# Performance work log

Hardware: AMD Instinct MI355X
Metric: run time of the kernel (lower is better)

Reference implementation:

```python
import jax, jax.numpy as jnp
import numpy as np

NUM_CLASSES = 91
BBOX_XFORM_CLIP = float(np.log(1000.0 / 16.0))
WX, WY, WW, WH = 10.0, 10.0, 5.0, 5.0  # torchvision BoxCoder weights
DETECTIONS_PER_IMG = 100


def _decode_boxes(reg, props):
    # reg: [P, 4*C], props: [P, 4] -> [P, C, 4]  (torchvision BoxCoder.decode)
    widths = props[:, 2] - props[:, 0]
    heights = props[:, 3] - props[:, 1]
    ctr_x = props[:, 0] + 0.5 * widths
    ctr_y = props[:, 1] + 0.5 * heights
    r = reg.reshape(reg.shape[0], -1, 4)
    dx = r[..., 0] / WX
    dy = r[..., 1] / WY
    dw = jnp.minimum(r[..., 2] / WW, BBOX_XFORM_CLIP)
    dh = jnp.minimum(r[..., 3] / WH, BBOX_XFORM_CLIP)
    pcx = dx * widths[:, None] + ctr_x[:, None]
    pcy = dy * heights[:, None] + ctr_y[:, None]
    pw = jnp.exp(dw) * widths[:, None]
    ph = jnp.exp(dh) * heights[:, None]
    return jnp.stack([pcx - 0.5 * pw, pcy - 0.5 * ph, pcx + 0.5 * pw, pcy + 0.5 * ph], axis=-1)


def _clip_boxes(boxes, h, w):
    x = jnp.clip(boxes[..., 0::2], 0.0, float(w))
    y = jnp.clip(boxes[..., 1::2], 0.0, float(h))
    return jnp.stack([x[..., 0], y[..., 0], x[..., 1], y[..., 1]], axis=-1)


def setup_inputs() -> dict:
    key = jax.random.key(0)
    k1, k2, k3, k4, k5 = jax.random.split(key, 5)
    B, P, C, FD = 8, 4096, NUM_CLASSES, 1024
    N = B * P
    class_logits = jax.random.normal(k1, (N, C), dtype=jnp.float32)
    box_regression = 0.5 * jax.random.normal(k2, (N, 4 * C), dtype=jnp.float32)
    # valid proposal boxes inside an 800x800 image: x1<x2, y1<y2
    xy = jax.random.uniform(k3, (N, 2), dtype=jnp.float32) * 700.0
    wh = jax.random.uniform(k4, (N, 2), dtype=jnp.float32) * 96.0 + 4.0
    proposals = jnp.concatenate([xy, xy + wh], axis=-1)
    box_features = jax.random.normal(k5, (N, FD), dtype=jnp.float32)
    return {"class_logits": class_logits, "box_regression": box_regression,
            "proposals": proposals, "box_features": box_features,
            "batch_size": B, "image_h": 800, "image_w": 800}


def reference(class_logits, box_regression, proposals, box_features, batch_size, image_h, image_w):
    B = int(batch_size)
    N = class_logits.shape[0]
    P = N // B
    lg = class_logits.reshape(B, P, NUM_CLASSES)
    rg = box_regression.reshape(B, P, 4 * NUM_CLASSES)
    pr = proposals.reshape(B, P, 4)
    ft = box_features.reshape(B, P, -1)

    def per_image(lg_i, rg_i, pr_i, ft_i):
        boxes = _decode_boxes(rg_i, pr_i)            # [P, C, 4]
        scores = jax.nn.softmax(lg_i, axis=-1)       # [P, C]
        boxes = _clip_boxes(boxes, image_h, image_w)
        boxes = boxes[:, 1:].reshape(-1, 4)          # drop background class -> [P*(C-1), 4]
        scores = scores[:, 1:].reshape(-1)
        # batched_nms with iou_threshold=1.0 never suppresses anything (IoU<=1 always),
        # so keep == indices sorted by score descending, truncated to detections_per_img.
        keep = jnp.argsort(-scores)[:DETECTIONS_PER_IMG]
        boxes = boxes / float(image_h)               # source divides by image_shape[0] only
        kept_boxes = boxes[keep]                     # [D, 4]
        feat_idx = keep // (NUM_CLASSES - 1)         # source: keep / (num_classes-1) int div
        kept_feats = ft_i[feat_idx]                  # [D, FD]
        return kept_boxes, kept_feats

    all_boxes, all_features = jax.vmap(per_image)(lg, rg, pr, ft)
    return all_boxes, all_features
```

## Files before the change

kernel.cpp:

```cpp
#include <hip/hip_runtime.h>
#include <hip/hip_bf16.h>

#define NCLS 91
#define NFG 90
#define NDET 100
#define FDIM 1024
#define CAP 4096
#define NBUK 4096
#define BBOX_CLIP 4.135166556742356f
#define K1_TPB 256
#define RPB 32
#define K2_TPB 1024

__global__ __launch_bounds__(K1_TPB) void k1_soft(
        const float* __restrict__ logits, float* __restrict__ rowoff,
        unsigned* __restrict__ maxk, int N) {
    int wave = threadIdx.x >> 6, lane = threadIdx.x & 63;
    int rowbase = blockIdx.x * RPB + wave * (RPB / 4);
    for (int it = 0; it < RPB / 4; it++) {
        long long row = rowbase + it;
        if (row >= N) return;
        const float* r = logits + row * NCLS;
        float l1 = r[lane];
        float l2 = (lane < NCLS - 64) ? r[64 + lane] : -INFINITY;
        float mf = fmaxf((lane == 0) ? -INFINITY : l1, l2);
        #pragma unroll
        for (int o = 32; o; o >>= 1) mf = fmaxf(mf, __shfl_xor(mf, o));
        float m = fmaxf(mf, __shfl(l1, 0));
        float e = expf(l1 - m) + ((lane < NCLS - 64) ? expf(l2 - m) : 0.0f);
        #pragma unroll
        for (int o = 32; o; o >>= 1) e += __shfl_xor(e, o);
        float off = m + logf(e);
        unsigned km = __float_as_uint(expf(mf - off));
        if (lane == 0) { rowoff[row] = off; maxk[row] = km; }
    }
}

__device__ __forceinline__ void find_threshold(const unsigned* hist,
                                               unsigned* wsum, unsigned* sh_lb,
                                               int tid, unsigned target) {
    unsigned local[16]; unsigned s = 0, run = 0;
    if (tid < 256) {
        #pragma unroll
        for (int i = 0; i < 16; i++) { local[i] = hist[tid * 16 + i]; s += local[i]; }
        run = s;
        #pragma unroll
        for (int off = 1; off < 64; off <<= 1) {
            unsigned v = __shfl_down(run, off);
            if ((tid & 63) + off < 64) run += v;
        }
        if ((tid & 63) == 0) wsum[tid >> 6] = run;
    }
    __syncthreads();
    if (tid < 256) {
        int w = tid >> 6;
        #pragma unroll
        for (int ww = 0; ww < 4; ww++) if (ww > w) run += wsum[ww];
        unsigned above = run - s;
        #pragma unroll
        for (int i = 15; i >= 0; i--) {
            unsigned prev = above; above += local[i];
            if (above >= target && prev < target)
                *sh_lb = ((unsigned)(tid * 16 + i)) << 20;
        }
    }
    __syncthreads();
}

__global__ __launch_bounds__(K2_TPB) void k2_select(
        const float* __restrict__ logits, const float* __restrict__ reg,
        const float* __restrict__ props,
        const int* __restrict__ pH, const int* __restrict__ pW,
        const float* __restrict__ rowoff, const unsigned* __restrict__ maxk,
        float* __restrict__ outBoxes, unsigned* __restrict__ keepRow, int P) {
    __shared__ unsigned long long cand[CAP];
    __shared__ unsigned long long cbuf[2048];
    __shared__ unsigned hist[NBUK];
    __shared__ unsigned wsum[4];
    __shared__ unsigned sh_lb, sh_lb2, sh_nhot, sh_ncand, sh_n2;

    const int img = blockIdx.x;
    const int tid = threadIdx.x;
    const unsigned* mk = maxk + (size_t)img * P;
    unsigned* hot = (unsigned*)cbuf;

    if (tid == 0) { sh_nhot = 0; sh_ncand = 0; sh_n2 = 0; sh_lb = 0; sh_lb2 = 0; }
    for (int b = tid; b < NBUK; b += K2_TPB) hist[b] = 0u;
    __syncthreads();

    for (int r = tid; r < P; r += K2_TPB) atomicAdd(&hist[mk[r] >> 20], 1u);
    __syncthreads();
    find_threshold(hist, wsum, &sh_lb, tid, NDET);
    const unsigned lb = sh_lb;
    const unsigned lbh = lb ? lb - 1 : 0;

    for (int r = tid; r < P; r += K2_TPB)
        if (mk[r] >= lbh) hot[atomicAdd(&sh_nhot, 1u)] = (unsigned)r;
    __syncthreads();
    const int nhot = (int)sh_nhot;

    const int wave = tid >> 6, lane = tid & 63;
    for (int i = wave; i < nhot; i += K2_TPB / 64) {
        int rl = (int)hot[i];
        long long row = (long long)img * P + rl;
        float off = rowoff[row];
        const float* r = logits + row * NCLS;
        float l1 = r[lane];
        float l2 = (lane < NCLS - 64) ? r[64 + lane] : -INFINITY;
        if (lane >= 1) {
            unsigned k = __float_as_uint(expf(l1 - off));
            if (k >= lb) {
                unsigned pos = atomicAdd(&sh_ncand, 1u);
                if (pos < CAP)
                    cand[pos] = ((unsigned long long)k << 32) |
                                (unsigned)(0xFFFFFFFFu - (unsigned)(rl * NFG + lane - 1));
            }
        }
        if (lane < NCLS - 64) {
            unsigned k = __float_as_uint(expf(l2 - off));
            if (k >= lb) {
                unsigned pos = atomicAdd(&sh_ncand, 1u);
                if (pos < CAP)
                    cand[pos] = ((unsigned long long)k << 32) |
                                (unsigned)(0xFFFFFFFFu - (unsigned)(rl * NFG + 63 + lane));
            }
        }
    }
    __syncthreads();
    unsigned cnt = sh_ncand; if (cnt > CAP) cnt = CAP;
    int n;

    if (cnt > 128) {
        for (int b = tid; b < NBUK; b += K2_TPB) hist[b] = 0u;
        __syncthreads();
        for (int i = tid; i < (int)cnt; i += K2_TPB)
            atomicAdd(&hist[(unsigned)(cand[i] >> 52)], 1u);
        __syncthreads();
        find_threshold(hist, wsum, &sh_lb2, tid, NDET);
        unsigned lb2 = sh_lb2;
        for (int i = tid; i < (int)cnt; i += K2_TPB) {
            unsigned long long k64 = cand[i];
            if ((unsigned)(k64 >> 32) >= lb2) {
                unsigned pos = atomicAdd(&sh_n2, 1u);
                if (pos < 2048) cbuf[pos] = k64;
            }
        }
        __syncthreads();
        unsigned cnt2 = sh_n2;
        if (cnt2 <= 2048) {
            cnt = cnt2;
            n = 128; while (n < (int)cnt) n <<= 1;
            for (int i = tid; i < n; i += K2_TPB)
                cand[i] = (i < (int)cnt) ? cbuf[i] : 0ULL;
            __syncthreads();
        } else {
            n = 128; while (n < (int)cnt) n <<= 1;
            for (int i = tid; i < n; i += K2_TPB) if (i >= (int)cnt) cand[i] = 0ULL;
            __syncthreads();
        }
    } else {
        n = 128;
        for (int i = tid; i < n; i += K2_TPB) if (i >= (int)cnt) cand[i] = 0ULL;
        __syncthreads();
    }

    for (int k = 2; k <= n; k <<= 1) {
        for (int j = k >> 1; j > 0; j >>= 1) {
            for (int i = tid; i < n; i += K2_TPB) {
                int ixj = i ^ j;
                if (ixj > i) {
                    bool up = ((i & k) == 0);
                    unsigned long long a = cand[i], b = cand[ixj];
                    if ((a > b) == up) { cand[i] = b; cand[ixj] = a; }
                }
            }
            __syncthreads();
        }
    }

    if (tid < NDET) {
        unsigned long long key = cand[n - 1 - tid];
        unsigned e = 0xFFFFFFFFu - (unsigned)(key & 0xFFFFFFFFull);
        int pr = e / NFG, cm = e - pr * NFG, c = cm + 1;
        long long rw = (long long)img * P + pr;
        float x1 = props[rw * 4 + 0], y1 = props[rw * 4 + 1];
        float x2 = props[rw * 4 + 2], y2 = props[rw * 4 + 3];
        float w = x2 - x1, hgt = y2 - y1;
        float cx = x1 + 0.5f * w, cy = y1 + 0.5f * hgt;
        const float* rr = reg + rw * (4 * NCLS) + 4 * c;
        float dx = rr[0] / 10.0f, dy = rr[1] / 10.0f;
        float dw = fminf(rr[2] / 5.0f, BBOX_CLIP);
        float dh = fminf(rr[3] / 5.0f, BBOX_CLIP);
        float pcx = dx * w + cx, pcy = dy * hgt + cy;
        float pw_ = expf(dw) * w, ph_ = expf(dh) * hgt;
        float bx1 = pcx - 0.5f * pw_, by1 = pcy - 0.5f * ph_;
        float bx2 = pcx + 0.5f * pw_, by2 = pcy + 0.5f * ph_;
        float W = (float)(*pW), H = (float)(*pH);
        bx1 = fminf(fmaxf(bx1, 0.0f), W);
        bx2 = fminf(fmaxf(bx2, 0.0f), W);
        by1 = fminf(fmaxf(by1, 0.0f), H);
        by2 = fminf(fmaxf(by2, 0.0f), H);
        int o = (img * NDET + tid) * 4;
        outBoxes[o + 0] = bx1 / H;
        outBoxes[o + 1] = by1 / H;
        outBoxes[o + 2] = bx2 / H;
        outBoxes[o + 3] = by2 / H;
        keepRow[img * NDET + tid] = (unsigned)rw;
    }
}

__global__ __launch_bounds__(256) void k3_feats(
        const float* __restrict__ feats, const unsigned* __restrict__ keepRow,
        float* __restrict__ outF) {
    int det = blockIdx.x;
    long long r = keepRow[det];
    const float4* src = (const float4*)(feats + r * FDIM);
    float4* dst = (float4*)(outF + (long long)det * FDIM);
    dst[threadIdx.x] = src[threadIdx.x];
}

extern "C" void kernel_launch(void* const* d_in, const int* in_sizes, int n_in,
                              void* d_out, int out_size, void* d_ws, size_t ws_size,
                              hipStream_t stream) {
    const float* logits = (const float*)d_in[0];
    const float* reg    = (const float*)d_in[1];
    const float* props  = (const float*)d_in[2];
    const float* feats  = (const float*)d_in[3];
    const int*   pH     = (const int*)d_in[5];
    const int*   pW     = (const int*)d_in[6];

    int N = in_sizes[0] / NCLS;
    int B = out_size / (NDET * (4 + FDIM));
    int P = N / B;

    char* ws = (char*)d_ws;
    float*    rowoff  = (float*)ws;
    unsigned* maxk    = (unsigned*)(rowoff + N);
    unsigned* keepRow = (unsigned*)(maxk + N);

    float* outBoxes = (float*)d_out;
    float* outFeats = outBoxes + (size_t)B * NDET * 4;

    k1_soft<<<(N + RPB - 1) / RPB, K1_TPB, 0, stream>>>(logits, rowoff, maxk, N);
    k2_select<<<B, K2_TPB, 0, stream>>>(logits, reg, props, pH, pW,
                                        rowoff, maxk, outBoxes, keepRow, P);
    k3_feats<<<B * NDET, 256, 0, stream>>>(feats, keepRow, outFeats);
}
```

Baseline: 224.2 us.

## Split per-image selection into multi-block collect and sort kernels with global histogram

The row-max histogram moves into the softmax kernel through global atomics, so the selection kernel no longer rebuilds it. Candidate collection is spread over 8 blocks per image that write into a global candidate buffer with global atomic counters. A separate per-image kernel then refines the threshold and sorts. This is meant to remove the serial per-image work done by only 8 blocks, at the cost of two extra launches (zeroing and the split), global atomics, and a candidate cap that can overflow.

```diff
diff --git a/kernel.cpp b/kernel.cpp
--- a/kernel.cpp
+++ b/kernel.cpp
@@ -1,20 +1,28 @@
 #include <hip/hip_runtime.h>
-#include <hip/hip_bf16.h>
 
 #define NCLS 91
 #define NFG 90
 #define NDET 100
 #define FDIM 1024
-#define CAP 4096
 #define NBUK 4096
+#define CAP_G 8192
+#define CAP_L 4096
+#define HOT_CAP 2048
 #define BBOX_CLIP 4.135166556742356f
 #define K1_TPB 256
 #define RPB 32
 #define K2_TPB 1024
+#define GPB 8
+
+__global__ __launch_bounds__(256) void k0_zero(unsigned* __restrict__ p, int n) {
+    int i = blockIdx.x * 256 + threadIdx.x;
+    if (i < n) p[i] = 0u;
+}
 
 __global__ __launch_bounds__(K1_TPB) void k1_soft(
         const float* __restrict__ logits, float* __restrict__ rowoff,
-        unsigned* __restrict__ maxk, int N) {
+        unsigned* __restrict__ maxk, unsigned* __restrict__ ghist,
+        int N, int P) {
     int wave = threadIdx.x >> 6, lane = threadIdx.x & 63;
     int rowbase = blockIdx.x * RPB + wave * (RPB / 4);
     for (int it = 0; it < RPB / 4; it++) {
@@ -32,7 +40,11 @@
         for (int o = 32; o; o >>= 1) e += __shfl_xor(e, o);
         float off = m + logf(e);
         unsigned km = __float_as_uint(expf(mf - off));
-        if (lane == 0) { rowoff[row] = off; maxk[row] = km; }
+        if (lane == 0) {
+            rowoff[row] = off; maxk[row] = km;
+            int img = (int)(row / P);
+            atomicAdd(&ghist[img * NBUK + (km >> 20)], 1u);
+        }
     }
 }
 
@@ -67,39 +79,36 @@
     __syncthreads();
 }
 
-__global__ __launch_bounds__(K2_TPB) void k2_select(
-        const float* __restrict__ logits, const float* __restrict__ reg,
-        const float* __restrict__ props,
-        const int* __restrict__ pH, const int* __restrict__ pW,
-        const float* __restrict__ rowoff, const unsigned* __restrict__ maxk,
-        float* __restrict__ outBoxes, unsigned* __restrict__ keepRow, int P) {
-    __shared__ unsigned long long cand[CAP];
-    __shared__ unsigned long long cbuf[2048];
-    __shared__ unsigned hist[NBUK];
+__global__ __launch_bounds__(K2_TPB) void k2a_collect(
+        const float* __restrict__ logits, const float* __restrict__ rowoff,
+        const unsigned* __restrict__ maxk, const unsigned* __restrict__ ghist,
+        unsigned long long* __restrict__ gcand, unsigned* __restrict__ gcnt,
+        int P) {
+    __shared__ unsigned hot[HOT_CAP];
     __shared__ unsigned wsum[4];
-    __shared__ unsigned sh_lb, sh_lb2, sh_nhot, sh_ncand, sh_n2;
-
-    const int img = blockIdx.x;
+    __shared__ unsigned sh_lb, sh_nhot;
+
+    const int img = blockIdx.x / GPB, sub = blockIdx.x % GPB;
     const int tid = threadIdx.x;
-    const unsigned* mk = maxk + (size_t)img * P;
-    unsigned* hot = (unsigned*)cbuf;
-
-    if (tid == 0) { sh_nhot = 0; sh_ncand = 0; sh_n2 = 0; sh_lb = 0; sh_lb2 = 0; }
-    for (int b = tid; b < NBUK; b += K2_TPB) hist[b] = 0u;
-    __syncthreads();
-
-    for (int r = tid; r < P; r += K2_TPB) atomicAdd(&hist[mk[r] >> 20], 1u);
-    __syncthreads();
-    find_threshold(hist, wsum, &sh_lb, tid, NDET);
+    if (tid == 0) { sh_lb = 0; sh_nhot = 0; }
+    find_threshold(ghist + (size_t)img * NBUK, wsum, &sh_lb, tid, NDET);
     const unsigned lb = sh_lb;
     const unsigned lbh = lb ? lb - 1 : 0;
 
-    for (int r = tid; r < P; r += K2_TPB)
-        if (mk[r] >= lbh) hot[atomicAdd(&sh_nhot, 1u)] = (unsigned)r;
-    __syncthreads();
-    const int nhot = (int)sh_nhot;
+    const int chunk = (P + GPB - 1) / GPB;
+    const int r0 = sub * chunk;
+    const int r1 = (r0 + chunk < P) ? (r0 + chunk) : P;
+    const unsigned* mk = maxk + (size_t)img * P;
+    for (int r = r0 + tid; r < r1; r += K2_TPB)
+        if (mk[r] >= lbh) {
+            unsigned p = atomicAdd(&sh_nhot, 1u);
+            if (p < HOT_CAP) hot[p] = (unsigned)r;
+        }
+    __syncthreads();
+    int nhot = (int)sh_nhot; if (nhot > HOT_CAP) nhot = HOT_CAP;
 
     const int wave = tid >> 6, lane = tid & 63;
+    unsigned long long* gc = gcand + (size_t)img * CAP_G;
     for (int i = wave; i < nhot; i += K2_TPB / 64) {
         int rl = (int)hot[i];
         long long row = (long long)img * P + rl;
@@ -110,59 +119,60 @@
         if (lane >= 1) {
             unsigned k = __float_as_uint(expf(l1 - off));
             if (k >= lb) {
-                unsigned pos = atomicAdd(&sh_ncand, 1u);
-                if (pos < CAP)
-                    cand[pos] = ((unsigned long long)k << 32) |
-                                (unsigned)(0xFFFFFFFFu - (unsigned)(rl * NFG + lane - 1));
+                unsigned pos = atomicAdd(&gcnt[img], 1u);
+                if (pos < CAP_G)
+                    gc[pos] = ((unsigned long long)k << 32) |
+                              (unsigned)(0xFFFFFFFFu - (unsigned)(rl * NFG + lane - 1));
             }
         }
         if (lane < NCLS - 64) {
             unsigned k = __float_as_uint(expf(l2 - off));
             if (k >= lb) {
-                unsigned pos = atomicAdd(&sh_ncand, 1u);
-                if (pos < CAP)
-                    cand[pos] = ((unsigned long long)k << 32) |
-                                (unsigned)(0xFFFFFFFFu - (unsigned)(rl * NFG + 63 + lane));
+                unsigned pos = atomicAdd(&gcnt[img], 1u);
+                if (pos < CAP_G)
+                    gc[pos] = ((unsigned long long)k << 32) |
+                              (unsigned)(0xFFFFFFFFu - (unsigned)(rl * NFG + 63 + lane));
             }
         }
     }
-    __syncthreads();
-    unsigned cnt = sh_ncand; if (cnt > CAP) cnt = CAP;
-    int n;
-
-    if (cnt > 128) {
-        for (int b = tid; b < NBUK; b += K2_TPB) hist[b] = 0u;
-        __syncthreads();
-        for (int i = tid; i < (int)cnt; i += K2_TPB)
-            atomicAdd(&hist[(unsigned)(cand[i] >> 52)], 1u);
-        __syncthreads();
-        find_threshold(hist, wsum, &sh_lb2, tid, NDET);
-        unsigned lb2 = sh_lb2;
-        for (int i = tid; i < (int)cnt; i += K2_TPB) {
-            unsigned long long k64 = cand[i];
-            if ((unsigned)(k64 >> 32) >= lb2) {
-                unsigned pos = atomicAdd(&sh_n2, 1u);
-                if (pos < 2048) cbuf[pos] = k64;
-            }
-        }
-        __syncthreads();
-        unsigned cnt2 = sh_n2;
-        if (cnt2 <= 2048) {
-            cnt = cnt2;
-            n = 128; while (n < (int)cnt) n <<= 1;
-            for (int i = tid; i < n; i += K2_TPB)
-                cand[i] = (i < (int)cnt) ? cbuf[i] : 0ULL;
-            __syncthreads();
-        } else {
-            n = 128; while (n < (int)cnt) n <<= 1;
-            for (int i = tid; i < n; i += K2_TPB) if (i >= (int)cnt) cand[i] = 0ULL;
-            __syncthreads();
-        }
-    } else {
-        n = 128;
-        for (int i = tid; i < n; i += K2_TPB) if (i >= (int)cnt) cand[i] = 0ULL;
-        __syncthreads();
-    }
+}
+
+__global__ __launch_bounds__(K2_TPB) void k2b_sort(
+        const float* __restrict__ reg, const float* __restrict__ props,
+        const int* __restrict__ pH, const int* __restrict__ pW,
+        const unsigned long long* __restrict__ gcand,
+        const unsigned* __restrict__ gcnt,
+        float* __restrict__ outBoxes, unsigned* __restrict__ keepRow, int P) {
+    __shared__ unsigned long long cand[CAP_L];
+    __shared__ unsigned hist[NBUK];
+    __shared__ unsigned wsum[4];
+    __shared__ unsigned sh_lb2, sh_n2;
+
+    const int img = blockIdx.x, tid = threadIdx.x;
+    if (tid == 0) { sh_lb2 = 0; sh_n2 = 0; }
+    for (int b = tid; b < NBUK; b += K2_TPB) hist[b] = 0u;
+    __syncthreads();
+
+    unsigned cnt = gcnt[img]; if (cnt > CAP_G) cnt = CAP_G;
+    const unsigned long long* gc = gcand + (size_t)img * CAP_G;
+
+    for (int i = tid; i < (int)cnt; i += K2_TPB)
+        atomicAdd(&hist[(unsigned)(gc[i] >> 52)], 1u);
+    __syncthreads();
+    find_threshold(hist, wsum, &sh_lb2, tid, NDET);
+    const unsigned lb2 = sh_lb2;
+    for (int i = tid; i < (int)cnt; i += K2_TPB) {
+        unsigned long long k64 = gc[i];
+        if ((unsigned)(k64 >> 32) >= lb2) {
+            unsigned pos = atomicAdd(&sh_n2, 1u);
+            if (pos < CAP_L) cand[pos] = k64;
+        }
+    }
+    __syncthreads();
+    unsigned cnt2 = sh_n2; if (cnt2 > CAP_L) cnt2 = CAP_L;
+    int n = 128; while (n < (int)cnt2) n <<= 1;
+    for (int i = tid; i < n; i += K2_TPB) if (i >= (int)cnt2) cand[i] = 0ULL;
+    __syncthreads();
 
     for (int k = 2; k <= n; k <<= 1) {
         for (int j = k >> 1; j > 0; j >>= 1) {
@@ -234,15 +244,23 @@
     int P = N / B;
 
     char* ws = (char*)d_ws;
-    float*    rowoff  = (float*)ws;
+    unsigned long long* gcand = (unsigned long long*)ws;
+    float*    rowoff  = (float*)(gcand + (size_t)B * CAP_G);
     unsigned* maxk    = (unsigned*)(rowoff + N);
     unsigned* keepRow = (unsigned*)(maxk + N);
+    unsigned* ghist   = keepRow + (size_t)B * NDET;
+    unsigned* gcnt    = ghist + (size_t)B * NBUK;
 
     float* outBoxes = (float*)d_out;
     float* outFeats = outBoxes + (size_t)B * NDET * 4;
 
-    k1_soft<<<(N + RPB - 1) / RPB, K1_TPB, 0, stream>>>(logits, rowoff, maxk, N);
-    k2_select<<<B, K2_TPB, 0, stream>>>(logits, reg, props, pH, pW,
-                                        rowoff, maxk, outBoxes, keepRow, P);
+    int nzero = B * NBUK + B;
+    k0_zero<<<(nzero + 255) / 256, 256, 0, stream>>>(ghist, nzero);
+    k1_soft<<<(N + RPB - 1) / RPB, K1_TPB, 0, stream>>>(logits, rowoff, maxk,
+                                                        ghist, N, P);
+    k2a_collect<<<B * GPB, K2_TPB, 0, stream>>>(logits, rowoff, maxk, ghist,
+                                                gcand, gcnt, P);
+    k2b_sort<<<B, K2_TPB, 0, stream>>>(reg, props, pH, pW, gcand, gcnt,
+                                       outBoxes, keepRow, P);
     k3_feats<<<B * NDET, 256, 0, stream>>>(feats, keepRow, outFeats);
 }
```

Result: slower. 265.2 us (+18.3%).

## Fuse softmax, selection and feature gather into one cooperative kernel

Applied to the files above, without the earlier changes.

Replaces the three separate kernel launches with a single cooperative kernel of 256 blocks of 1024 threads, using grid-wide syncs between the softmax-stats phase, the per-image top-k selection phase and the feature gather phase. The aim is to remove launch overhead and inter-kernel gaps. In exchange, every block must reserve the large shared-memory footprint of the selection phase even during softmax, which limits occupancy. The selection phase still runs on only B blocks while the rest wait at a grid barrier, and a cooperative launch may fail if the grid cannot be co-resident.

```diff
diff --git a/kernel.cpp b/kernel.cpp
--- a/kernel.cpp
+++ b/kernel.cpp
@@ -1,5 +1,7 @@
 #include <hip/hip_runtime.h>
-#include <hip/hip_bf16.h>
+#include <hip/hip_cooperative_groups.h>
+
+namespace cg = cooperative_groups;
 
 #define NCLS 91
 #define NFG 90
@@ -8,33 +10,8 @@
 #define CAP 4096
 #define NBUK 4096
 #define BBOX_CLIP 4.135166556742356f
-#define K1_TPB 256
-#define RPB 32
-#define K2_TPB 1024
-
-__global__ __launch_bounds__(K1_TPB) void k1_soft(
-        const float* __restrict__ logits, float* __restrict__ rowoff,
-        unsigned* __restrict__ maxk, int N) {
-    int wave = threadIdx.x >> 6, lane = threadIdx.x & 63;
-    int rowbase = blockIdx.x * RPB + wave * (RPB / 4);
-    for (int it = 0; it < RPB / 4; it++) {
-        long long row = rowbase + it;
-        if (row >= N) return;
-        const float* r = logits + row * NCLS;
-        float l1 = r[lane];
-        float l2 = (lane < NCLS - 64) ? r[64 + lane] : -INFINITY;
-        float mf = fmaxf((lane == 0) ? -INFINITY : l1, l2);
-        #pragma unroll
-        for (int o = 32; o; o >>= 1) mf = fmaxf(mf, __shfl_xor(mf, o));
-        float m = fmaxf(mf, __shfl(l1, 0));
-        float e = expf(l1 - m) + ((lane < NCLS - 64) ? expf(l2 - m) : 0.0f);
-        #pragma unroll
-        for (int o = 32; o; o >>= 1) e += __shfl_xor(e, o);
-        float off = m + logf(e);
-        unsigned km = __float_as_uint(expf(mf - off));
-        if (lane == 0) { rowoff[row] = off; maxk[row] = km; }
-    }
-}
+#define TPB 1024
+#define NBLK 256
 
 __device__ __forceinline__ void find_threshold(const unsigned* hist,
                                                unsigned* wsum, unsigned* sh_lb,
@@ -67,156 +44,185 @@
     __syncthreads();
 }
 
-__global__ __launch_bounds__(K2_TPB) void k2_select(
+__global__ __launch_bounds__(TPB) void fused_all(
         const float* __restrict__ logits, const float* __restrict__ reg,
-        const float* __restrict__ props,
+        const float* __restrict__ props, const float* __restrict__ feats,
         const int* __restrict__ pH, const int* __restrict__ pW,
-        const float* __restrict__ rowoff, const unsigned* __restrict__ maxk,
-        float* __restrict__ outBoxes, unsigned* __restrict__ keepRow, int P) {
+        float* __restrict__ rowoff, unsigned* __restrict__ maxk,
+        unsigned* __restrict__ keepRow,
+        float* __restrict__ outBoxes, float* __restrict__ outFeats,
+        int N, int P, int B) {
     __shared__ unsigned long long cand[CAP];
     __shared__ unsigned long long cbuf[2048];
     __shared__ unsigned hist[NBUK];
     __shared__ unsigned wsum[4];
     __shared__ unsigned sh_lb, sh_lb2, sh_nhot, sh_ncand, sh_n2;
 
-    const int img = blockIdx.x;
+    cg::grid_group grid = cg::this_grid();
     const int tid = threadIdx.x;
-    const unsigned* mk = maxk + (size_t)img * P;
-    unsigned* hot = (unsigned*)cbuf;
-
-    if (tid == 0) { sh_nhot = 0; sh_ncand = 0; sh_n2 = 0; sh_lb = 0; sh_lb2 = 0; }
-    for (int b = tid; b < NBUK; b += K2_TPB) hist[b] = 0u;
-    __syncthreads();
-
-    for (int r = tid; r < P; r += K2_TPB) atomicAdd(&hist[mk[r] >> 20], 1u);
-    __syncthreads();
-    find_threshold(hist, wsum, &sh_lb, tid, NDET);
-    const unsigned lb = sh_lb;
-    const unsigned lbh = lb ? lb - 1 : 0;
-
-    for (int r = tid; r < P; r += K2_TPB)
-        if (mk[r] >= lbh) hot[atomicAdd(&sh_nhot, 1u)] = (unsigned)r;
-    __syncthreads();
-    const int nhot = (int)sh_nhot;
-
     const int wave = tid >> 6, lane = tid & 63;
-    for (int i = wave; i < nhot; i += K2_TPB / 64) {
-        int rl = (int)hot[i];
-        long long row = (long long)img * P + rl;
-        float off = rowoff[row];
-        const float* r = logits + row * NCLS;
-        float l1 = r[lane];
-        float l2 = (lane < NCLS - 64) ? r[64 + lane] : -INFINITY;
-        if (lane >= 1) {
-            unsigned k = __float_as_uint(expf(l1 - off));
-            if (k >= lb) {
-                unsigned pos = atomicAdd(&sh_ncand, 1u);
-                if (pos < CAP)
-                    cand[pos] = ((unsigned long long)k << 32) |
-                                (unsigned)(0xFFFFFFFFu - (unsigned)(rl * NFG + lane - 1));
-            }
-        }
-        if (lane < NCLS - 64) {
-            unsigned k = __float_as_uint(expf(l2 - off));
-            if (k >= lb) {
-                unsigned pos = atomicAdd(&sh_ncand, 1u);
-                if (pos < CAP)
-                    cand[pos] = ((unsigned long long)k << 32) |
-                                (unsigned)(0xFFFFFFFFu - (unsigned)(rl * NFG + 63 + lane));
-            }
-        }
-    }
-    __syncthreads();
-    unsigned cnt = sh_ncand; if (cnt > CAP) cnt = CAP;
-    int n;
-
-    if (cnt > 128) {
-        for (int b = tid; b < NBUK; b += K2_TPB) hist[b] = 0u;
-        __syncthreads();
-        for (int i = tid; i < (int)cnt; i += K2_TPB)
-            atomicAdd(&hist[(unsigned)(cand[i] >> 52)], 1u);
-        __syncthreads();
-        find_threshold(hist, wsum, &sh_lb2, tid, NDET);
-        unsigned lb2 = sh_lb2;
-        for (int i = tid; i < (int)cnt; i += K2_TPB) {
-            unsigned long long k64 = cand[i];
-            if ((unsigned)(k64 >> 32) >= lb2) {
-                unsigned pos = atomicAdd(&sh_n2, 1u);
-                if (pos < 2048) cbuf[pos] = k64;
-            }
-        }
-        __syncthreads();
-        unsigned cnt2 = sh_n2;
-        if (cnt2 <= 2048) {
-            cnt = cnt2;
-            n = 128; while (n < (int)cnt) n <<= 1;
-            for (int i = tid; i < n; i += K2_TPB)
-                cand[i] = (i < (int)cnt) ? cbuf[i] : 0ULL;
-            __syncthreads();
+
+    {
+        const int nwaves = NBLK * (TPB >> 6);
+        const int gw = blockIdx.x * (TPB >> 6) + wave;
+        for (long long row = gw; row < N; row += nwaves) {
+            const float* r = logits + row * NCLS;
+            float l1 = r[lane];
+            float l2 = (lane < NCLS - 64) ? r[64 + lane] : -INFINITY;
+            float mf = fmaxf((lane == 0) ? -INFINITY : l1, l2);
+            #pragma unroll
+            for (int o = 32; o; o >>= 1) mf = fmaxf(mf, __shfl_xor(mf, o));
+            float m = fmaxf(mf, __shfl(l1, 0));
+            float e = expf(l1 - m) + ((lane < NCLS - 64) ? expf(l2 - m) : 0.0f);
+            #pragma unroll
+            for (int o = 32; o; o >>= 1) e += __shfl_xor(e, o);
+            float off = m + logf(e);
+            unsigned km = __float_as_uint(expf(mf - off));
+            if (lane == 0) { rowoff[row] = off; maxk[row] = km; }
+        }
+    }
+    grid.sync();
+
+    if (blockIdx.x < (unsigned)B) {
+        const int img = blockIdx.x;
+        const unsigned* mk = maxk + (size_t)img * P;
+        unsigned* hot = (unsigned*)cbuf;
+
+        if (tid == 0) { sh_nhot = 0; sh_ncand = 0; sh_n2 = 0; sh_lb = 0; sh_lb2 = 0; }
+        for (int b = tid; b < NBUK; b += TPB) hist[b] = 0u;
+        __syncthreads();
+
+        for (int r = tid; r < P; r += TPB) atomicAdd(&hist[mk[r] >> 20], 1u);
+        __syncthreads();
+        find_threshold(hist, wsum, &sh_lb, tid, NDET);
+        const unsigned lb = sh_lb;
+        const unsigned lbh = lb ? lb - 1 : 0;
+
+        for (int r = tid; r < P; r += TPB)
+            if (mk[r] >= lbh) hot[atomicAdd(&sh_nhot, 1u)] = (unsigned)r;
+        __syncthreads();
+        const int nhot = (int)sh_nhot;
+
+        for (int i = wave; i < nhot; i += TPB / 64) {
+            int rl = (int)hot[i];
+            long long row = (long long)img * P + rl;
+            float off = rowoff[row];
+            const float* r = logits + row * NCLS;
+            float l1 = r[lane];
+            float l2 = (lane < NCLS - 64) ? r[64 + lane] : -INFINITY;
+            if (lane >= 1) {
+                unsigned k = __float_as_uint(expf(l1 - off));
+                if (k >= lb) {
+                    unsigned pos = atomicAdd(&sh_ncand, 1u);
+                    if (pos < CAP)
+                        cand[pos] = ((unsigned long long)k << 32) |
+                                    (unsigned)(0xFFFFFFFFu - (unsigned)(rl * NFG + lane - 1));
+                }
+            }
+            if (lane < NCLS - 64) {
+                unsigned k = __float_as_uint(expf(l2 - off));
+                if (k >= lb) {
+                    unsigned pos = atomicAdd(&sh_ncand, 1u);
+                    if (pos < CAP)
+                        cand[pos] = ((unsigned long long)k << 32) |
+                                    (unsigned)(0xFFFFFFFFu - (unsigned)(rl * NFG + 63 + lane));
+                }
+            }
+        }
+        __syncthreads();
+        unsigned cnt = sh_ncand; if (cnt > CAP) cnt = CAP;
+        int n;
+
+        if (cnt > 128) {
+            for (int b = tid; b < NBUK; b += TPB) hist[b] = 0u;
+            __syncthreads();
+            for (int i = tid; i < (int)cnt; i += TPB)
+                atomicAdd(&hist[(unsigned)(cand[i] >> 52)], 1u);
+            __syncthreads();
+            find_threshold(hist, wsum, &sh_lb2, tid, NDET);
+            unsigned lb2 = sh_lb2;
+            for (int i = tid; i < (int)cnt; i += TPB) {
+                unsigned long long k64 = cand[i];
+                if ((unsigned)(k64 >> 32) >= lb2) {
+                    unsigned pos = atomicAdd(&sh_n2, 1u);
+                    if (pos < 2048) cbuf[pos] = k64;
+                }
+            }
+            __syncthreads();
+            unsigned cnt2 = sh_n2;
+            if (cnt2 <= 2048) {
+                cnt = cnt2;
+                n = 128; while (n < (int)cnt) n <<= 1;
+                for (int i = tid; i < n; i += TPB)
+                    cand[i] = (i < (int)cnt) ? cbuf[i] : 0ULL;
+                __syncthreads();
+            } else {
+                n = 128; while (n < (int)cnt) n <<= 1;
+                for (int i = tid; i < n; i += TPB) if (i >= (int)cnt) cand[i] = 0ULL;
+                __syncthreads();
+            }
         } else {
-            n = 128; while (n < (int)cnt) n <<= 1;
-            for (int i = tid; i < n; i += K2_TPB) if (i >= (int)cnt) cand[i] = 0ULL;
-            __syncthreads();
-        }
-    } else {
-        n = 128;
-        for (int i = tid; i < n; i += K2_TPB) if (i >= (int)cnt) cand[i] = 0ULL;
-        __syncthreads();
-    }
-
-    for (int k = 2; k <= n; k <<= 1) {
-        for (int j = k >> 1; j > 0; j >>= 1) {
-            for (int i = tid; i < n; i += K2_TPB) {
-                int ixj = i ^ j;
-                if (ixj > i) {
-                    bool up = ((i & k) == 0);
-                    unsigned long long a = cand[i], b = cand[ixj];
-                    if ((a > b) == up) { cand[i] = b; cand[ixj] = a; }
-                }
-            }
-            __syncthreads();
-        }
-    }
-
-    if (tid < NDET) {
-        unsigned long long key = cand[n - 1 - tid];
-        unsigned e = 0xFFFFFFFFu - (unsigned)(key & 0xFFFFFFFFull);
-        int pr = e / NFG, cm = e - pr * NFG, c = cm + 1;
-        long long rw = (long long)img * P + pr;
-        float x1 = props[rw * 4 + 0], y1 = props[rw * 4 + 1];
-        float x2 = props[rw * 4 + 2], y2 = props[rw * 4 + 3];
-        float w = x2 - x1, hgt = y2 - y1;
-        float cx = x1 + 0.5f * w, cy = y1 + 0.5f * hgt;
-        const float* rr = reg + rw * (4 * NCLS) + 4 * c;
-        float dx = rr[0] / 10.0f, dy = rr[1] / 10.0f;
-        float dw = fminf(rr[2] / 5.0f, BBOX_CLIP);
-        float dh = fminf(rr[3] / 5.0f, BBOX_CLIP);
-        float pcx = dx * w + cx, pcy = dy * hgt + cy;
-        float pw_ = expf(dw) * w, ph_ = expf(dh) * hgt;
-        float bx1 = pcx - 0.5f * pw_, by1 = pcy - 0.5f * ph_;
-        float bx2 = pcx + 0.5f * pw_, by2 = pcy + 0.5f * ph_;
-        float W = (float)(*pW), H = (float)(*pH);
-        bx1 = fminf(fmaxf(bx1, 0.0f), W);
-        bx2 = fminf(fmaxf(bx2, 0.0f), W);
-        by1 = fminf(fmaxf(by1, 0.0f), H);
-        by2 = fminf(fmaxf(by2, 0.0f), H);
-        int o = (img * NDET + tid) * 4;
-        outBoxes[o + 0] = bx1 / H;
-        outBoxes[o + 1] = by1 / H;
-        outBoxes[o + 2] = bx2 / H;
-        outBoxes[o + 3] = by2 / H;
-        keepRow[img * NDET + tid] = (unsigned)rw;
-    }
-}
-
-__global__ __launch_bounds__(256) void k3_feats(
-        const float* __restrict__ feats, const unsigned* __restrict__ keepRow,
-        float* __restrict__ outF) {
-    int det = blockIdx.x;
-    long long r = keepRow[det];
-    const float4* src = (const float4*)(feats + r * FDIM);
-    float4* dst = (float4*)(outF + (long long)det * FDIM);
-    dst[threadIdx.x] = src[threadIdx.x];
+            n = 128;
+            for (int i = tid; i < n; i += TPB) if (i >= (int)cnt) cand[i] = 0ULL;
+            __syncthreads();
+        }
+
+        for (int k = 2; k <= n; k <<= 1) {
+            for (int j = k >> 1; j > 0; j >>= 1) {
+                for (int i = tid; i < n; i += TPB) {
+                    int ixj = i ^ j;
+                    if (ixj > i) {
+                        bool up = ((i & k) == 0);
+                        unsigned long long a = cand[i], b = cand[ixj];
+                        if ((a > b) == up) { cand[i] = b; cand[ixj] = a; }
+                    }
+                }
+                __syncthreads();
+            }
+        }
+
+        if (tid < NDET) {
+            unsigned long long key = cand[n - 1 - tid];
+            unsigned e = 0xFFFFFFFFu - (unsigned)(key & 0xFFFFFFFFull);
+            int pr = e / NFG, cm = e - pr * NFG, c = cm + 1;
+            long long rw = (long long)img * P + pr;
+            float x1 = props[rw * 4 + 0], y1 = props[rw * 4 + 1];
+            float x2 = props[rw * 4 + 2], y2 = props[rw * 4 + 3];
+            float w = x2 - x1, hgt = y2 - y1;
+            float cx = x1 + 0.5f * w, cy = y1 + 0.5f * hgt;
+            const float* rr = reg + rw * (4 * NCLS) + 4 * c;
+            float dx = rr[0] / 10.0f, dy = rr[1] / 10.0f;
+            float dw = fminf(rr[2] / 5.0f, BBOX_CLIP);
+            float dh = fminf(rr[3] / 5.0f, BBOX_CLIP);
+            float pcx = dx * w + cx, pcy = dy * hgt + cy;
+            float pw_ = expf(dw) * w, ph_ = expf(dh) * hgt;
+            float bx1 = pcx - 0.5f * pw_, by1 = pcy - 0.5f * ph_;
+            float bx2 = pcx + 0.5f * pw_, by2 = pcy + 0.5f * ph_;
+            float W = (float)(*pW), H = (float)(*pH);
+            bx1 = fminf(fmaxf(bx1, 0.0f), W);
+            bx2 = fminf(fmaxf(bx2, 0.0f), W);
+            by1 = fminf(fmaxf(by1, 0.0f), H);
+            by2 = fminf(fmaxf(by2, 0.0f), H);
+            int o = (img * NDET + tid) * 4;
+            outBoxes[o + 0] = bx1 / H;
+            outBoxes[o + 1] = by1 / H;
+            outBoxes[o + 2] = bx2 / H;
+            outBoxes[o + 3] = by2 / H;
+            keepRow[img * NDET + tid] = (unsigned)rw;
+        }
+    }
+    grid.sync();
+
+    {
+        const int ndet = B * NDET;
+        const int grp = tid >> 8, sub = tid & 255;
+        for (int det = (int)blockIdx.x * 4 + grp; det < ndet; det += NBLK * 4) {
+            long long r = keepRow[det];
+            const float4* src = (const float4*)(feats + r * FDIM);
+            float4* dst = (float4*)(outFeats + (long long)det * FDIM);
+            dst[sub] = src[sub];
+        }
+    }
 }
 
 extern "C" void kernel_launch(void* const* d_in, const int* in_sizes, int n_in,
@@ -241,8 +247,9 @@
     float* outBoxes = (float*)d_out;
     float* outFeats = outBoxes + (size_t)B * NDET * 4;
 
-    k1_soft<<<(N + RPB - 1) / RPB, K1_TPB, 0, stream>>>(logits, rowoff, maxk, N);
-    k2_select<<<B, K2_TPB, 0, stream>>>(logits, reg, props, pH, pW,
-                                        rowoff, maxk, outBoxes, keepRow, P);
-    k3_feats<<<B * NDET, 256, 0, stream>>>(feats, keepRow, outFeats);
+    void* args[] = { &logits, &reg, &props, &feats, &pH, &pW,
+                     &rowoff, &maxk, &keepRow, &outBoxes, &outFeats,
+                     &N, &P, &B };
+    hipLaunchCooperativeKernel((const void*)fused_all, dim3(NBLK), dim3(TPB),
+                               args, 0, stream);
 }
```

After: 289.6 us. +29.2%, slower.

## Split per-image selection across blocks with last-block-done merge and fused feature gather

Applied to the files above, without the earlier changes.

The select kernel now runs 16 blocks per image, each scanning a slice of proposal rows for candidates and appending them to a global per-image buffer via atomic counters. The last block to finish (tracked by an atomic done counter) performs the final threshold, sort and box decode, then copies the kept feature rows itself, which removes the separate gather kernel launch. This targets the low parallelism of one block per image, at the cost of redundant histogram work in every block, global-memory traffic for candidates, and a serialized tail on one block per image.

```diff
diff --git a/kernel.cpp b/kernel.cpp
--- a/kernel.cpp
+++ b/kernel.cpp
@@ -1,20 +1,25 @@
 #include <hip/hip_runtime.h>
-#include <hip/hip_bf16.h>
 
 #define NCLS 91
 #define NFG 90
 #define NDET 100
 #define FDIM 1024
-#define CAP 4096
 #define NBUK 4096
+#define CAP_G 16384
+#define CAP_L 4096
+#define HOT_CAP 512
 #define BBOX_CLIP 4.135166556742356f
 #define K1_TPB 256
 #define RPB 32
 #define K2_TPB 1024
+#define GPB 16
 
 __global__ __launch_bounds__(K1_TPB) void k1_soft(
         const float* __restrict__ logits, float* __restrict__ rowoff,
-        unsigned* __restrict__ maxk, int N) {
+        unsigned* __restrict__ maxk, unsigned* __restrict__ counters,
+        int N, int B) {
+    if (blockIdx.x == 0 && threadIdx.x < (unsigned)(2 * B))
+        counters[threadIdx.x] = 0u;
     int wave = threadIdx.x >> 6, lane = threadIdx.x & 63;
     int rowbase = blockIdx.x * RPB + wave * (RPB / 4);
     for (int it = 0; it < RPB / 4; it++) {
@@ -67,39 +72,46 @@
     __syncthreads();
 }
 
-__global__ __launch_bounds__(K2_TPB) void k2_select(
+__global__ __launch_bounds__(K2_TPB) void k2_all(
         const float* __restrict__ logits, const float* __restrict__ reg,
-        const float* __restrict__ props,
+        const float* __restrict__ props, const float* __restrict__ feats,
         const int* __restrict__ pH, const int* __restrict__ pW,
         const float* __restrict__ rowoff, const unsigned* __restrict__ maxk,
-        float* __restrict__ outBoxes, unsigned* __restrict__ keepRow, int P) {
-    __shared__ unsigned long long cand[CAP];
-    __shared__ unsigned long long cbuf[2048];
+        unsigned long long* __restrict__ gcand, unsigned* __restrict__ gcnt,
+        unsigned* __restrict__ gdone,
+        float* __restrict__ outBoxes, float* __restrict__ outFeats, int P) {
+    __shared__ unsigned long long cand[CAP_L];
     __shared__ unsigned hist[NBUK];
+    __shared__ unsigned hot[HOT_CAP];
+    __shared__ unsigned keepL[NDET];
     __shared__ unsigned wsum[4];
-    __shared__ unsigned sh_lb, sh_lb2, sh_nhot, sh_ncand, sh_n2;
-
-    const int img = blockIdx.x;
-    const int tid = threadIdx.x;
+    __shared__ unsigned sh_lb, sh_lb2, sh_nhot, sh_nc, sh_base, sh_done, sh_n2;
+
+    const int img = blockIdx.x / GPB, sub = blockIdx.x % GPB;
+    const int tid = threadIdx.x, wave = tid >> 6, lane = tid & 63;
+
+    if (tid == 0) { sh_lb = 0; sh_lb2 = 0; sh_nhot = 0; sh_nc = 0; sh_n2 = 0; }
+    for (int b = tid; b < NBUK; b += K2_TPB) hist[b] = 0u;
+    __syncthreads();
+
     const unsigned* mk = maxk + (size_t)img * P;
-    unsigned* hot = (unsigned*)cbuf;
-
-    if (tid == 0) { sh_nhot = 0; sh_ncand = 0; sh_n2 = 0; sh_lb = 0; sh_lb2 = 0; }
-    for (int b = tid; b < NBUK; b += K2_TPB) hist[b] = 0u;
-    __syncthreads();
-
     for (int r = tid; r < P; r += K2_TPB) atomicAdd(&hist[mk[r] >> 20], 1u);
     __syncthreads();
     find_threshold(hist, wsum, &sh_lb, tid, NDET);
     const unsigned lb = sh_lb;
     const unsigned lbh = lb ? lb - 1 : 0;
 
-    for (int r = tid; r < P; r += K2_TPB)
-        if (mk[r] >= lbh) hot[atomicAdd(&sh_nhot, 1u)] = (unsigned)r;
-    __syncthreads();
-    const int nhot = (int)sh_nhot;
-
-    const int wave = tid >> 6, lane = tid & 63;
+    const int chunk = (P + GPB - 1) / GPB;
+    const int r0 = sub * chunk;
+    const int r1 = (r0 + chunk < P) ? (r0 + chunk) : P;
+    for (int r = r0 + tid; r < r1; r += K2_TPB)
+        if (mk[r] >= lbh) {
+            unsigned hp = atomicAdd(&sh_nhot, 1u);
+            if (hp < HOT_CAP) hot[hp] = (unsigned)r;
+        }
+    __syncthreads();
+    int nhot = (int)sh_nhot; if (nhot > HOT_CAP) nhot = HOT_CAP;
+
     for (int i = wave; i < nhot; i += K2_TPB / 64) {
         int rl = (int)hot[i];
         long long row = (long long)img * P + rl;
@@ -110,8 +122,8 @@
         if (lane >= 1) {
             unsigned k = __float_as_uint(expf(l1 - off));
             if (k >= lb) {
-                unsigned pos = atomicAdd(&sh_ncand, 1u);
-                if (pos < CAP)
+                unsigned pos = atomicAdd(&sh_nc, 1u);
+                if (pos < CAP_L)
                     cand[pos] = ((unsigned long long)k << 32) |
                                 (unsigned)(0xFFFFFFFFu - (unsigned)(rl * NFG + lane - 1));
             }
@@ -119,48 +131,56 @@
         if (lane < NCLS - 64) {
             unsigned k = __float_as_uint(expf(l2 - off));
             if (k >= lb) {
-                unsigned pos = atomicAdd(&sh_ncand, 1u);
-                if (pos < CAP)
+                unsigned pos = atomicAdd(&sh_nc, 1u);
+                if (pos < CAP_L)
                     cand[pos] = ((unsigned long long)k << 32) |
                                 (unsigned)(0xFFFFFFFFu - (unsigned)(rl * NFG + 63 + lane));
             }
         }
     }
     __syncthreads();
-    unsigned cnt = sh_ncand; if (cnt > CAP) cnt = CAP;
+    unsigned nc = sh_nc; if (nc > CAP_L) nc = CAP_L;
+
+    if (tid == 0) sh_base = atomicAdd(&gcnt[img], nc);
+    __syncthreads();
+    unsigned base = sh_base;
+    unsigned long long* gc = gcand + (size_t)img * CAP_G;
+    for (unsigned i = tid; i < nc; i += K2_TPB)
+        if (base + i < CAP_G) gc[base + i] = cand[i];
+    __threadfence();
+    __syncthreads();
+    if (tid == 0) sh_done = atomicAdd(&gdone[img], 1u);
+    __syncthreads();
+    if (sh_done != GPB - 1) return;
+
+    __threadfence();
+    __syncthreads();
+    unsigned cnt = gcnt[img]; if (cnt > CAP_G) cnt = CAP_G;
+
+    for (int b = tid; b < NBUK; b += K2_TPB) hist[b] = 0u;
+    __syncthreads();
     int n;
-
     if (cnt > 128) {
-        for (int b = tid; b < NBUK; b += K2_TPB) hist[b] = 0u;
-        __syncthreads();
         for (int i = tid; i < (int)cnt; i += K2_TPB)
-            atomicAdd(&hist[(unsigned)(cand[i] >> 52)], 1u);
+            atomicAdd(&hist[(unsigned)(gc[i] >> 52)], 1u);
         __syncthreads();
         find_threshold(hist, wsum, &sh_lb2, tid, NDET);
         unsigned lb2 = sh_lb2;
         for (int i = tid; i < (int)cnt; i += K2_TPB) {
-            unsigned long long k64 = cand[i];
+            unsigned long long k64 = gc[i];
             if ((unsigned)(k64 >> 32) >= lb2) {
                 unsigned pos = atomicAdd(&sh_n2, 1u);
-                if (pos < 2048) cbuf[pos] = k64;
-            }
-        }
-        __syncthreads();
-        unsigned cnt2 = sh_n2;
-        if (cnt2 <= 2048) {
-            cnt = cnt2;
-            n = 128; while (n < (int)cnt) n <<= 1;
-            for (int i = tid; i < n; i += K2_TPB)
-                cand[i] = (i < (int)cnt) ? cbuf[i] : 0ULL;
-            __syncthreads();
-        } else {
-            n = 128; while (n < (int)cnt) n <<= 1;
-            for (int i = tid; i < n; i += K2_TPB) if (i >= (int)cnt) cand[i] = 0ULL;
-            __syncthreads();
-        }
+                if (pos < CAP_L) cand[pos] = k64;
+            }
+        }
+        __syncthreads();
+        unsigned c2 = sh_n2; if (c2 > CAP_L) c2 = CAP_L;
+        n = 128; while (n < (int)c2) n <<= 1;
+        for (int i = tid; i < n; i += K2_TPB) if (i >= (int)c2) cand[i] = 0ULL;
+        __syncthreads();
     } else {
         n = 128;
-        for (int i = tid; i < n; i += K2_TPB) if (i >= (int)cnt) cand[i] = 0ULL;
+        for (int i = tid; i < n; i += K2_TPB) cand[i] = (i < (int)cnt) ? gc[i] : 0ULL;
         __syncthreads();
     }
 
@@ -205,18 +225,19 @@
         outBoxes[o + 1] = by1 / H;
         outBoxes[o + 2] = bx2 / H;
         outBoxes[o + 3] = by2 / H;
-        keepRow[img * NDET + tid] = (unsigned)rw;
-    }
-}
-
-__global__ __launch_bounds__(256) void k3_feats(
-        const float* __restrict__ feats, const unsigned* __restrict__ keepRow,
-        float* __restrict__ outF) {
-    int det = blockIdx.x;
-    long long r = keepRow[det];
-    const float4* src = (const float4*)(feats + r * FDIM);
-    float4* dst = (float4*)(outF + (long long)det * FDIM);
-    dst[threadIdx.x] = src[threadIdx.x];
+        keepL[tid] = (unsigned)rw;
+    }
+    __syncthreads();
+
+    {
+        const int grp = tid >> 8, subl = tid & 255;
+        for (int d = grp; d < NDET; d += 4) {
+            long long r = keepL[d];
+            const float4* src = (const float4*)(feats + r * FDIM);
+            float4* dst = (float4*)(outFeats + ((long long)img * NDET + d) * FDIM);
+            dst[subl] = src[subl];
+        }
+    }
 }
 
 extern "C" void kernel_launch(void* const* d_in, const int* in_sizes, int n_in,
@@ -234,15 +255,18 @@
     int P = N / B;
 
     char* ws = (char*)d_ws;
-    float*    rowoff  = (float*)ws;
-    unsigned* maxk    = (unsigned*)(rowoff + N);
-    unsigned* keepRow = (unsigned*)(maxk + N);
+    unsigned long long* gcand = (unsigned long long*)ws;
+    float*    rowoff = (float*)(gcand + (size_t)B * CAP_G);
+    unsigned* maxk   = (unsigned*)(rowoff + N);
+    unsigned* gcnt   = (unsigned*)(maxk + N);
+    unsigned* gdone  = gcnt + B;
 
     float* outBoxes = (float*)d_out;
     float* outFeats = outBoxes + (size_t)B * NDET * 4;
 
-    k1_soft<<<(N + RPB - 1) / RPB, K1_TPB, 0, stream>>>(logits, rowoff, maxk, N);
-    k2_select<<<B, K2_TPB, 0, stream>>>(logits, reg, props, pH, pW,
-                                        rowoff, maxk, outBoxes, keepRow, P);
-    k3_feats<<<B * NDET, 256, 0, stream>>>(feats, keepRow, outFeats);
-}
+    k1_soft<<<(N + RPB - 1) / RPB, K1_TPB, 0, stream>>>(logits, rowoff, maxk,
+                                                        gcnt, N, B);
+    k2_all<<<B * GPB, K2_TPB, 0, stream>>>(logits, reg, props, feats, pH, pW,
+                                           rowoff, maxk, gcand, gcnt, gdone,
+                                           outBoxes, outFeats, P);
+}
```

New measurement: 273.2 us. 1.22x slower.
